# Kernel optimization log

Hardware: AMD Instinct MI355X
Metric: run time of the kernel (lower is better)

The kernel has to match this reference:

```python
import jax, jax.numpy as jnp
import numpy as np

SEQ, ATTN_LEN, C_IN, PS, DIM, LAYERS, HEADS, MLP = 10, 3, 48, 1, 48, 2, 8, 192


def setup_inputs() -> dict:
    key = jax.random.key(0)
    ks = jax.random.split(key, 10)
    B, H, W = 8, 64, 64
    s = 0.02
    f32 = jnp.float32
    return {
        "x": jax.random.normal(ks[0], (B, SEQ, C_IN, H, W), f32),
        "qkv_w": jax.random.normal(ks[1], (LAYERS, DIM, 3 * DIM), f32) * s,
        "qkv_b": jnp.zeros((LAYERS, 3 * DIM), f32),
        "proj_w": jax.random.normal(ks[2], (LAYERS, DIM, DIM), f32) * s,
        "proj_b": jnp.zeros((LAYERS, DIM), f32),
        "ff1_w": jax.random.normal(ks[3], (LAYERS, DIM, MLP), f32) * s,
        "ff1_b": jnp.zeros((LAYERS, MLP), f32),
        "ff2_w": jax.random.normal(ks[4], (LAYERS, MLP, DIM), f32) * s,
        "ff2_b": jnp.zeros((LAYERS, DIM), f32),
        "dw_w": jax.random.normal(ks[5], (2 * C_IN, 1, 3, 3), f32) * s,
        "dw_b": jnp.zeros((2 * C_IN,), f32),
        "ln_g": jnp.ones((2 * C_IN,), f32),
        "ln_b": jnp.zeros((2 * C_IN,), f32),
        "pw1_w": jax.random.normal(ks[6], (2 * C_IN, 8 * C_IN), f32) * s,
        "pw1_b": jnp.zeros((8 * C_IN,), f32),
        "pw2_w": jax.random.normal(ks[7], (8 * C_IN, C_IN), f32) * s,
        "pw2_b": jnp.zeros((C_IN,), f32),
        "sc_w": jax.random.normal(ks[8], (C_IN, 2 * C_IN), f32) * s,
        "sc_b": jnp.zeros((C_IN,), f32),
    }


def reference(x, qkv_w, qkv_b, proj_w, proj_b, ff1_w, ff1_b, ff2_w, ff2_b,
              dw_w, dw_b, ln_g, ln_b, pw1_w, pw1_b, pw2_w, pw2_b, sc_w, sc_b):
    B, C, F, H, W = x.shape
    # patchify (patch_size=1): (b, c, f, h, w) -> (b*h*w, c, f)
    t = x.transpose(0, 3, 4, 1, 2).reshape(B * H * W, C, F)
    # banded mask: True (disallowed) where |i-j| > attn_length//2
    nb = ATTN_LEN // 2
    idx = jnp.arange(C)
    mask = jnp.abs(idx[:, None] - idx[None, :]) > nb  # (C, C)
    neg = -jnp.finfo(t.dtype).max
    hd = DIM // HEADS
    scale = hd ** -0.5
    for l in range(LAYERS):
        # self-attention; NOTE: source computes scores = k @ q^T and softmaxes
        # over the query axis (faithful to original, not standard attention).
        qkv = (t @ qkv_w[l] + qkv_b[l]).reshape(B * H * W, C, 3, HEADS, hd)
        q, k, v = qkv[:, :, 0], qkv[:, :, 1], qkv[:, :, 2]  # (N, C, HEADS, hd)
        attn = jnp.einsum('nihd,njhd->nhij', k, q) * scale  # (N, HEADS, C, C)
        attn = jax.nn.softmax(jnp.where(mask, neg, attn), axis=-1)
        o = jnp.einsum('nhij,njhd->nihd', attn, v).reshape(B * H * W, C, DIM)
        t = t + (o @ proj_w[l] + proj_b[l])  # residual
        # feed-forward (GELU exact, as torch nn.GELU)
        h1 = jax.nn.gelu(t @ ff1_w[l] + ff1_b[l], approximate=False)
        t = t + (h1 @ ff2_w[l] + ff2_b[l])  # residual
    # unpatchify back to (B, C, F, H, W)
    y = t.reshape(B, H, W, C, F).transpose(0, 3, 4, 1, 2)
    # context_dropout is a no-op in eval with rate 0.0
    # concat original + context features along channels: (B*C, 2F, H, W)
    cat = jnp.concatenate([x.reshape(-1, F, H, W), y.reshape(-1, F, H, W)], axis=1)
    # ConvNeXt block: depthwise 3x3 -> channel LN -> pw expand -> GELU -> pw -> + 1x1 shortcut
    z = jax.lax.conv_general_dilated(cat, dw_w, (1, 1), 'SAME',
                                     feature_group_count=2 * F,
                                     dimension_numbers=('NCHW', 'OIHW', 'NCHW'))
    z = z + dw_b[None, :, None, None]
    z = z.transpose(0, 2, 3, 1)  # NHWC
    mu = z.mean(-1, keepdims=True)
    var = ((z - mu) ** 2).mean(-1, keepdims=True)
    z = (z - mu) / jnp.sqrt(var + 1e-6) * ln_g + ln_b
    z = jax.nn.gelu(z @ pw1_w + pw1_b, approximate=False) @ pw2_w + pw2_b
    z = z.transpose(0, 3, 1, 2)  # back to NCHW, F channels
    sc = jnp.einsum('nchw,oc->nohw', cat, sc_w) + sc_b[None, :, None, None]
    return (sc + z).reshape(B, C, F, H, W)
```

## Files before the change

kernel.cpp:

```cpp
#include <hip/hip_runtime.h>
#include <math.h>

#define THREADS 256


#define LKS 49

__global__ __launch_bounds__(64, 3) void ka2_transformer(
    const float* __restrict__ x,
    const float* __restrict__ qkv_w, const float* __restrict__ qkv_b,
    const float* __restrict__ proj_w, const float* __restrict__ proj_b,
    const float* __restrict__ ff1_w, const float* __restrict__ ff1_b,
    const float* __restrict__ ff2_w, const float* __restrict__ ff2_b,
    float* __restrict__ t_out)
{
    __shared__ float tl[64 * LKS];
    const int lane = threadIdx.x;

    const int nb  = gridDim.x;
    const int q8  = nb >> 3, r8 = nb & 7;
    const int xcd = blockIdx.x & 7, idx = blockIdx.x >> 3;
    const int wg  = (xcd < r8) ? xcd * (q8 + 1) + idx
                               : r8 * (q8 + 1) + (xcd - r8) * q8 + idx;

    const int s = lane / 10;
    const int c = lane - s * 10;
    const int g = wg * 6 + s;
    const bool act = (lane < 60) && (g < 32768);
    const int b   = g >> 12;
    const int pix = g & 4095;

    float* tr = tl + lane * LKS;

    if (act) {
        const float* xp = x + ((size_t)(b * 480 + c * 48)) * 4096 + pix;
        #pragma unroll
        for (int f = 0; f < 48; ++f) tr[f] = xp[(size_t)f * 4096];
    } else {
        #pragma unroll
        for (int f = 0; f < 48; ++f) tr[f] = 0.f;
    }

    const float scale = 0.4082482904638631f;
    const float NEG = -3.4e38f;

    for (int l = 0; l < 2; ++l) {
        const float* qw  = qkv_w + l * 6912;
        const float* qb  = qkv_b + l * 144;
        const float* pw  = proj_w + l * 2304;
        const float* pb  = proj_b + l * 48;
        const float* f1w = ff1_w + l * 9216;
        const float* f1b = ff1_b + l * 192;
        const float* f2w = ff2_w + l * 9216;
        const float* f2b = ff2_b + l * 48;

        float pacc[48];
        #pragma unroll
        for (int o = 0; o < 48; ++o) pacc[o] = 0.f;

        for (int h = 0; h < 8; ++h) {
            float qa[6], ka[6], va[6];
            #pragma unroll
            for (int d = 0; d < 6; ++d) { qa[d] = 0.f; ka[d] = 0.f; va[d] = 0.f; }

            for (int k = 0; k < 48; ++k) {
                const float tk = tr[k];
                const float* wr = qw + k * 144 + h * 6;
                #pragma unroll
                for (int d = 0; d < 6; ++d) {
                    qa[d] += tk * wr[d];
                    ka[d] += tk * wr[48 + d];
                    va[d] += tk * wr[96 + d];
                }
            }
            #pragma unroll
            for (int d = 0; d < 6; ++d) {
                qa[d] += qb[h * 6 + d];
                ka[d] += qb[48 + h * 6 + d];
                va[d] += qb[96 + h * 6 + d];
            }

            float qm[6], qp[6], vm[6], vp[6];
            #pragma unroll
            for (int d = 0; d < 6; ++d) {
                qm[d] = __shfl_up(qa[d], 1);
                qp[d] = __shfl_down(qa[d], 1);
                vm[d] = __shfl_up(va[d], 1);
                vp[d] = __shfl_down(va[d], 1);
            }
            float s0 = 0.f, sm = 0.f, sp = 0.f;
            #pragma unroll
            for (int d = 0; d < 6; ++d) {
                s0 += ka[d] * qa[d];
                sm += ka[d] * qm[d];
                sp += ka[d] * qp[d];
            }
            s0 *= scale; sm *= scale; sp *= scale;
            if (c == 0) sm = NEG;
            if (c == 9) sp = NEG;
            const float mx = fmaxf(s0, fmaxf(sm, sp));
            const float em = expf(sm - mx), e0 = expf(s0 - mx), ep = expf(sp - mx);
            const float inv = 1.0f / (em + e0 + ep);

            #pragma unroll
            for (int d = 0; d < 6; ++d) {
                const float ov = (em * vm[d] + e0 * va[d] + ep * vp[d]) * inv;
                const float* wr = pw + (h * 6 + d) * 48;
                #pragma unroll
                for (int o = 0; o < 48; ++o) pacc[o] += ov * wr[o];
            }
        }
        #pragma unroll
        for (int f = 0; f < 48; ++f) tr[f] += pacc[f] + pb[f];

        float facc[48];
        #pragma unroll
        for (int o = 0; o < 48; ++o) facc[o] = 0.f;

        for (int cc = 0; cc < 8; ++cc) {
            float ha[24];
            #pragma unroll
            for (int j = 0; j < 24; ++j) ha[j] = 0.f;

            for (int k = 0; k < 48; ++k) {
                const float tk = tr[k];
                const float* wr = f1w + k * 192 + cc * 24;
                #pragma unroll
                for (int j = 0; j < 24; ++j) ha[j] += tk * wr[j];
            }
            #pragma unroll
            for (int j = 0; j < 24; ++j) {
                float v = ha[j] + f1b[cc * 24 + j];
                ha[j] = 0.5f * v * (1.f + erff(v * 0.70710678118654752f));
            }
            #pragma unroll
            for (int j = 0; j < 24; ++j) {
                const float hj = ha[j];
                const float* wr = f2w + (cc * 24 + j) * 48;
                #pragma unroll
                for (int o = 0; o < 48; ++o) facc[o] += hj * wr[o];
            }
        }
        #pragma unroll
        for (int f = 0; f < 48; ++f) tr[f] += facc[f] + f2b[f];
    }

    if (act) {
        float* dst = t_out + (size_t)g * 480 + c * 48;
        #pragma unroll
        for (int u = 0; u < 12; ++u) {
            float4 v;
            v.x = tr[u * 4]; v.y = tr[u * 4 + 1];
            v.z = tr[u * 4 + 2]; v.w = tr[u * 4 + 3];
            *(float4*)(dst + u * 4) = v;
        }
    }
}

__global__ __launch_bounds__(THREADS) void kb_conv(
    const float* __restrict__ x, const float* __restrict__ t_in,
    const float* __restrict__ dw_w, const float* __restrict__ dw_b,
    float* __restrict__ z0)
{
    __shared__ float ct[100 * 97];
    const int tid = threadIdx.x;
    const int blk = blockIdx.x;
    const int n = blk >> 6;
    const int tile = blk & 63;
    const int th0 = (tile >> 3) << 3;
    const int tw0 = (tile & 7) << 3;
    const int b = n / 10, c = n % 10;

    for (int idx = tid; idx < 4800; idx += THREADS) {
        int f = idx / 100, p = idx % 100;
        int py = p / 10, px = p % 10;
        int gh = th0 + py - 1, gw = tw0 + px - 1;
        float v = 0.f;
        if ((unsigned)gh < 64u && (unsigned)gw < 64u)
            v = x[((size_t)n * 48 + f) * 4096 + gh * 64 + gw];
        ct[p * 97 + f] = v;
    }
    for (int idx = tid; idx < 4800; idx += THREADS) {
        int p = idx / 48, f = idx % 48;
        int py = p / 10, px = p % 10;
        int gh = th0 + py - 1, gw = tw0 + px - 1;
        float v = 0.f;
        if ((unsigned)gh < 64u && (unsigned)gw < 64u)
            v = t_in[(size_t)(b * 4096 + gh * 64 + gw) * 480 + c * 48 + f];
        ct[p * 97 + 48 + f] = v;
    }
    __syncthreads();

    #pragma unroll 4
    for (int it = 0; it < 24; ++it) {
        int oidx = tid + it * THREADS;
        int pxl = oidx / 96, ch = oidx % 96;
        int py = pxl >> 3, pxx = pxl & 7;
        const float* wp = dw_w + ch * 9;
        float acc = dw_b[ch];
        #pragma unroll
        for (int dy = 0; dy < 3; ++dy)
            #pragma unroll
            for (int dx = 0; dx < 3; ++dx)
                acc += ct[((py + dy) * 10 + pxx + dx) * 97 + ch] * wp[dy * 3 + dx];
        z0[((size_t)n * 4096 + (th0 + py) * 64 + (tw0 + pxx)) * 96 + ch] = acc;
    }
}

__global__ __launch_bounds__(THREADS, 3) void kc_mlp(
    const float* __restrict__ x, const float* __restrict__ t_in,
    const float* __restrict__ z0,
    const float* __restrict__ ln_g, const float* __restrict__ ln_b,
    const float* __restrict__ pw1_w, const float* __restrict__ pw1_b,
    const float* __restrict__ pw2_w, const float* __restrict__ pw2_b,
    const float* __restrict__ sc_w, const float* __restrict__ sc_b,
    float* __restrict__ out)
{
    __shared__ float zb[64 * 100];
    __shared__ float hb[64 * 100];
    const int tid = threadIdx.x;
    const int blk = blockIdx.x;
    const int n   = blk >> 6;
    const int hw0 = (blk & 63) << 6;
    const size_t pixbase = (size_t)n * 4096 + hw0;

    for (int idx = tid; idx < 1536; idx += THREADS) {
        float4 v = *(const float4*)(z0 + pixbase * 96 + (size_t)idx * 4);
        int p = idx / 24, c0 = (idx % 24) * 4;
        *(float4*)(&zb[p * 100 + c0]) = v;
    }
    __syncthreads();

    if (tid < 64) {
        float* r = zb + tid * 100;
        float mu = 0.f;
        #pragma unroll
        for (int k = 0; k < 96; ++k) mu += r[k];
        mu *= (1.f / 96.f);
        float var = 0.f;
        #pragma unroll
        for (int k = 0; k < 96; ++k) { float d = r[k] - mu; var += d * d; }
        var *= (1.f / 96.f);
        float rs = rsqrtf(var + 1e-6f);
        #pragma unroll
        for (int k = 0; k < 96; ++k) r[k] = (r[k] - mu) * rs * ln_g[k] + ln_b[k];
    }
    __syncthreads();

    const int pxg = tid >> 4;
    const int sub = tid & 15;
    const int f0  = sub * 3;

    float facc[4][3];
    #pragma unroll
    for (int r = 0; r < 4; ++r)
        #pragma unroll
        for (int c = 0; c < 3; ++c) facc[r][c] = pw2_b[f0 + c];

    for (int jc = 0; jc < 4; ++jc) {
        {
            const int j0 = jc * 96 + sub * 6;
            const float* zr = zb + pxg * 400;
            float h[4][6] = {};
            for (int k = 0; k < 96; k += 4) {
                float4 a0 = *(const float4*)(zr + k);
                float4 a1 = *(const float4*)(zr + 100 + k);
                float4 a2 = *(const float4*)(zr + 200 + k);
                float4 a3 = *(const float4*)(zr + 300 + k);
                #pragma unroll
                for (int kk = 0; kk < 4; ++kk) {
                    const float* wr = pw1_w + (k + kk) * 384 + j0;
                    const float e0 = (&a0.x)[kk], e1 = (&a1.x)[kk], e2 = (&a2.x)[kk], e3 = (&a3.x)[kk];
                    #pragma unroll
                    for (int c = 0; c < 6; ++c) {
                        const float w = wr[c];
                        h[0][c] += e0 * w; h[1][c] += e1 * w;
                        h[2][c] += e2 * w; h[3][c] += e3 * w;
                    }
                }
            }
            #pragma unroll
            for (int r = 0; r < 4; ++r)
                #pragma unroll
                for (int c = 0; c < 6; ++c) {
                    float v = h[r][c] + pw1_b[j0 + c];
                    v = 0.5f * v * (1.f + erff(v * 0.70710678118654752f));
                    hb[(pxg * 4 + r) * 100 + sub * 6 + c] = v;
                }
        }
        __syncthreads();

        {
            const float* hr = hb + pxg * 400;
            for (int k = 0; k < 96; k += 4) {
                float4 a0 = *(const float4*)(hr + k);
                float4 a1 = *(const float4*)(hr + 100 + k);
                float4 a2 = *(const float4*)(hr + 200 + k);
                float4 a3 = *(const float4*)(hr + 300 + k);
                #pragma unroll
                for (int kk = 0; kk < 4; ++kk) {
                    const float* wr = pw2_w + (jc * 96 + k + kk) * 48 + f0;
                    const float w0 = wr[0], w1 = wr[1], w2 = wr[2];
                    const float e0 = (&a0.x)[kk], e1 = (&a1.x)[kk], e2 = (&a2.x)[kk], e3 = (&a3.x)[kk];
                    facc[0][0] += e0 * w0; facc[0][1] += e0 * w1; facc[0][2] += e0 * w2;
                    facc[1][0] += e1 * w0; facc[1][1] += e1 * w1; facc[1][2] += e1 * w2;
                    facc[2][0] += e2 * w0; facc[2][1] += e2 * w1; facc[2][2] += e2 * w2;
                    facc[3][0] += e3 * w0; facc[3][1] += e3 * w1; facc[3][2] += e3 * w2;
                }
            }
        }
        __syncthreads();
    }

    for (int idx = tid; idx < 768; idx += THREADS) {
        int ch = idx >> 4, p0 = (idx & 15) << 2;
        float4 v = *(const float4*)(x + ((size_t)n * 48 + ch) * 4096 + hw0 + p0);
        zb[(p0 + 0) * 100 + ch] = v.x; zb[(p0 + 1) * 100 + ch] = v.y;
        zb[(p0 + 2) * 100 + ch] = v.z; zb[(p0 + 3) * 100 + ch] = v.w;
    }
    {
        const size_t tb = ((size_t)(n / 10) * 4096 + hw0);
        const int coff = (n % 10) * 48;
        for (int idx = tid; idx < 768; idx += THREADS) {
            int p = idx / 12, u0 = (idx % 12) * 4;
            float4 v = *(const float4*)(t_in + (tb + p) * 480 + coff + u0);
            *(float4*)(&zb[p * 100 + 48 + u0]) = v;
        }
    }
    __syncthreads();

    {
        const float* cr = zb + pxg * 400;
        for (int k = 0; k < 96; k += 4) {
            float4 a0 = *(const float4*)(cr + k);
            float4 a1 = *(const float4*)(cr + 100 + k);
            float4 a2 = *(const float4*)(cr + 200 + k);
            float4 a3 = *(const float4*)(cr + 300 + k);
            float4 w0 = *(const float4*)(sc_w + (f0 + 0) * 96 + k);
            float4 w1 = *(const float4*)(sc_w + (f0 + 1) * 96 + k);
            float4 w2 = *(const float4*)(sc_w + (f0 + 2) * 96 + k);
            #pragma unroll
            for (int kk = 0; kk < 4; ++kk) {
                const float e0 = (&a0.x)[kk], e1 = (&a1.x)[kk], e2 = (&a2.x)[kk], e3 = (&a3.x)[kk];
                const float q0 = (&w0.x)[kk], q1 = (&w1.x)[kk], q2 = (&w2.x)[kk];
                facc[0][0] += e0 * q0; facc[0][1] += e0 * q1; facc[0][2] += e0 * q2;
                facc[1][0] += e1 * q0; facc[1][1] += e1 * q1; facc[1][2] += e1 * q2;
                facc[2][0] += e2 * q0; facc[2][1] += e2 * q1; facc[2][2] += e2 * q2;
                facc[3][0] += e3 * q0; facc[3][1] += e3 * q1; facc[3][2] += e3 * q2;
            }
        }
    }
    __syncthreads();

    #pragma unroll
    for (int r = 0; r < 4; ++r)
        #pragma unroll
        for (int c = 0; c < 3; ++c)
            hb[(f0 + c) * 66 + pxg * 4 + r] = facc[r][c] + sc_b[f0 + c];
    __syncthreads();
    for (int idx = tid; idx < 768; idx += THREADS) {
        int f = idx / 16, p0 = (idx % 16) * 4;
        float4 v;
        v.x = hb[f * 66 + p0]; v.y = hb[f * 66 + p0 + 1];
        v.z = hb[f * 66 + p0 + 2]; v.w = hb[f * 66 + p0 + 3];
        *(float4*)(out + ((size_t)n * 48 + f) * 4096 + hw0 + p0) = v;
    }
}

extern "C" void kernel_launch(void* const* d_in, const int* in_sizes, int n_in,
                              void* d_out, int out_size, void* d_ws, size_t ws_size,
                              hipStream_t stream) {
    const float* x      = (const float*)d_in[0];
    const float* qkv_w  = (const float*)d_in[1];
    const float* qkv_b  = (const float*)d_in[2];
    const float* proj_w = (const float*)d_in[3];
    const float* proj_b = (const float*)d_in[4];
    const float* ff1_w  = (const float*)d_in[5];
    const float* ff1_b  = (const float*)d_in[6];
    const float* ff2_w  = (const float*)d_in[7];
    const float* ff2_b  = (const float*)d_in[8];
    const float* dw_w   = (const float*)d_in[9];
    const float* dw_b   = (const float*)d_in[10];
    const float* ln_g   = (const float*)d_in[11];
    const float* ln_b   = (const float*)d_in[12];
    const float* pw1_w  = (const float*)d_in[13];
    const float* pw1_b  = (const float*)d_in[14];
    const float* pw2_w  = (const float*)d_in[15];
    const float* pw2_b  = (const float*)d_in[16];
    const float* sc_w   = (const float*)d_in[17];
    const float* sc_b   = (const float*)d_in[18];
    float* out = (float*)d_out;

    float* t_out = (float*)d_ws;
    float* z0    = t_out + 15728640ull;

    ka2_transformer<<<5462, 64, 0, stream>>>(x, qkv_w, qkv_b, proj_w, proj_b,
                                             ff1_w, ff1_b, ff2_w, ff2_b, t_out);
    kb_conv<<<5120, THREADS, 0, stream>>>(x, t_out, dw_w, dw_b, z0);
    kc_mlp<<<5120, THREADS, 0, stream>>>(x, t_out, z0, ln_g, ln_b,
                                         pw1_w, pw1_b, pw2_w, pw2_b, sc_w, sc_b, out);
}
```

Measured before the change: 1.981 ms.

## Rewrite pointwise MLP kernel as one-pixel-per-lane single-wave blocks with register accumulators

The ConvNeXt MLP kernel now uses 64-thread blocks where each lane owns one pixel. Each lane keeps all 48 output accumulators in registers and streams the hidden layer through in 24-wide chunks, so the shared hidden buffer and the barriers inside the loop are gone. Weights are read with wave-uniform addresses, which should let them become scalar or broadcast loads. A small pre-kernel transposes the shortcut weights into a device global so they can be read the same way. The cost is heavy register pressure (48 plus 24 accumulators) and only one wave per block, which may lower occupancy or cause spills.

```diff
diff --git a/kernel.cpp b/kernel.cpp
--- a/kernel.cpp
+++ b/kernel.cpp
@@ -3,6 +3,16 @@
 
 #define THREADS 256
 
+
+__device__ float g_scwT[96 * 48];
+
+__global__ void kt_transpose(const float* __restrict__ sc_w) {
+    int i = threadIdx.x + blockIdx.x * 256;
+    if (i < 48 * 96) {
+        int o = i / 96, k = i % 96;
+        g_scwT[k * 48 + o] = sc_w[o * 96 + k];
+    }
+}
 
 #define LKS 49
 
@@ -207,163 +217,126 @@
     }
 }
 
-__global__ __launch_bounds__(THREADS, 3) void kc_mlp(
+#define ZS 100
+
+__global__ __launch_bounds__(64) void kc2_mlp(
     const float* __restrict__ x, const float* __restrict__ t_in,
     const float* __restrict__ z0,
     const float* __restrict__ ln_g, const float* __restrict__ ln_b,
     const float* __restrict__ pw1_w, const float* __restrict__ pw1_b,
     const float* __restrict__ pw2_w, const float* __restrict__ pw2_b,
-    const float* __restrict__ sc_w, const float* __restrict__ sc_b,
+    const float* __restrict__ sc_b,
     float* __restrict__ out)
 {
-    __shared__ float zb[64 * 100];
-    __shared__ float hb[64 * 100];
-    const int tid = threadIdx.x;
+    __shared__ float zb[64 * ZS];
+    const int lane = threadIdx.x;
     const int blk = blockIdx.x;
     const int n   = blk >> 6;
     const int hw0 = (blk & 63) << 6;
     const size_t pixbase = (size_t)n * 4096 + hw0;
 
-    for (int idx = tid; idx < 1536; idx += THREADS) {
+    for (int idx = lane; idx < 1536; idx += 64) {
         float4 v = *(const float4*)(z0 + pixbase * 96 + (size_t)idx * 4);
         int p = idx / 24, c0 = (idx % 24) * 4;
-        *(float4*)(&zb[p * 100 + c0]) = v;
+        *(float4*)(&zb[p * ZS + c0]) = v;
     }
     __syncthreads();
 
-    if (tid < 64) {
-        float* r = zb + tid * 100;
+    float* zr = zb + lane * ZS;
+
+    {
         float mu = 0.f;
-        #pragma unroll
-        for (int k = 0; k < 96; ++k) mu += r[k];
+        for (int k = 0; k < 96; k += 4) {
+            float4 v = *(const float4*)(zr + k);
+            mu += v.x; mu += v.y; mu += v.z; mu += v.w;
+        }
         mu *= (1.f / 96.f);
         float var = 0.f;
-        #pragma unroll
-        for (int k = 0; k < 96; ++k) { float d = r[k] - mu; var += d * d; }
+        for (int k = 0; k < 96; k += 4) {
+            float4 v = *(const float4*)(zr + k);
+            float d0 = v.x - mu, d1 = v.y - mu, d2 = v.z - mu, d3 = v.w - mu;
+            var += d0 * d0; var += d1 * d1; var += d2 * d2; var += d3 * d3;
+        }
         var *= (1.f / 96.f);
         float rs = rsqrtf(var + 1e-6f);
-        #pragma unroll
-        for (int k = 0; k < 96; ++k) r[k] = (r[k] - mu) * rs * ln_g[k] + ln_b[k];
-    }
+        for (int k = 0; k < 96; k += 4) {
+            float4 v = *(const float4*)(zr + k);
+            v.x = (v.x - mu) * rs * ln_g[k + 0] + ln_b[k + 0];
+            v.y = (v.y - mu) * rs * ln_g[k + 1] + ln_b[k + 1];
+            v.z = (v.z - mu) * rs * ln_g[k + 2] + ln_b[k + 2];
+            v.w = (v.w - mu) * rs * ln_g[k + 3] + ln_b[k + 3];
+            *(float4*)(zr + k) = v;
+        }
+    }
+
+    float facc[48];
+    #pragma unroll
+    for (int o = 0; o < 48; ++o) facc[o] = pw2_b[o];
+
+    for (int jc = 0; jc < 16; ++jc) {
+        const int j0 = jc * 24;
+        float ha[24];
+        #pragma unroll
+        for (int j = 0; j < 24; ++j) ha[j] = 0.f;
+
+        for (int k = 0; k < 96; k += 4) {
+            float4 a = *(const float4*)(zr + k);
+            #pragma unroll
+            for (int kk = 0; kk < 4; ++kk) {
+                const float e = (&a.x)[kk];
+                const float* wr = pw1_w + (k + kk) * 384 + j0;
+                #pragma unroll
+                for (int j = 0; j < 24; ++j) ha[j] += e * wr[j];
+            }
+        }
+        #pragma unroll
+        for (int j = 0; j < 24; ++j) {
+            float v = ha[j] + pw1_b[j0 + j];
+            ha[j] = 0.5f * v * (1.f + erff(v * 0.70710678118654752f));
+        }
+        #pragma unroll
+        for (int j = 0; j < 24; ++j) {
+            const float hj = ha[j];
+            const float* wr = pw2_w + (j0 + j) * 48;
+            #pragma unroll
+            for (int o = 0; o < 48; ++o) facc[o] += hj * wr[o];
+        }
+    }
+
     __syncthreads();
-
-    const int pxg = tid >> 4;
-    const int sub = tid & 15;
-    const int f0  = sub * 3;
-
-    float facc[4][3];
-    #pragma unroll
-    for (int r = 0; r < 4; ++r)
-        #pragma unroll
-        for (int c = 0; c < 3; ++c) facc[r][c] = pw2_b[f0 + c];
-
-    for (int jc = 0; jc < 4; ++jc) {
-        {
-            const int j0 = jc * 96 + sub * 6;
-            const float* zr = zb + pxg * 400;
-            float h[4][6] = {};
-            for (int k = 0; k < 96; k += 4) {
-                float4 a0 = *(const float4*)(zr + k);
-                float4 a1 = *(const float4*)(zr + 100 + k);
-                float4 a2 = *(const float4*)(zr + 200 + k);
-                float4 a3 = *(const float4*)(zr + 300 + k);
-                #pragma unroll
-                for (int kk = 0; kk < 4; ++kk) {
-                    const float* wr = pw1_w + (k + kk) * 384 + j0;
-                    const float e0 = (&a0.x)[kk], e1 = (&a1.x)[kk], e2 = (&a2.x)[kk], e3 = (&a3.x)[kk];
-                    #pragma unroll
-                    for (int c = 0; c < 6; ++c) {
-                        const float w = wr[c];
-                        h[0][c] += e0 * w; h[1][c] += e1 * w;
-                        h[2][c] += e2 * w; h[3][c] += e3 * w;
-                    }
-                }
-            }
-            #pragma unroll
-            for (int r = 0; r < 4; ++r)
-                #pragma unroll
-                for (int c = 0; c < 6; ++c) {
-                    float v = h[r][c] + pw1_b[j0 + c];
-                    v = 0.5f * v * (1.f + erff(v * 0.70710678118654752f));
-                    hb[(pxg * 4 + r) * 100 + sub * 6 + c] = v;
-                }
-        }
-        __syncthreads();
-
-        {
-            const float* hr = hb + pxg * 400;
-            for (int k = 0; k < 96; k += 4) {
-                float4 a0 = *(const float4*)(hr + k);
-                float4 a1 = *(const float4*)(hr + 100 + k);
-                float4 a2 = *(const float4*)(hr + 200 + k);
-                float4 a3 = *(const float4*)(hr + 300 + k);
-                #pragma unroll
-                for (int kk = 0; kk < 4; ++kk) {
-                    const float* wr = pw2_w + (jc * 96 + k + kk) * 48 + f0;
-                    const float w0 = wr[0], w1 = wr[1], w2 = wr[2];
-                    const float e0 = (&a0.x)[kk], e1 = (&a1.x)[kk], e2 = (&a2.x)[kk], e3 = (&a3.x)[kk];
-                    facc[0][0] += e0 * w0; facc[0][1] += e0 * w1; facc[0][2] += e0 * w2;
-                    facc[1][0] += e1 * w0; facc[1][1] += e1 * w1; facc[1][2] += e1 * w2;
-                    facc[2][0] += e2 * w0; facc[2][1] += e2 * w1; facc[2][2] += e2 * w2;
-                    facc[3][0] += e3 * w0; facc[3][1] += e3 * w1; facc[3][2] += e3 * w2;
-                }
-            }
-        }
-        __syncthreads();
-    }
-
-    for (int idx = tid; idx < 768; idx += THREADS) {
+    for (int idx = lane; idx < 768; idx += 64) {
         int ch = idx >> 4, p0 = (idx & 15) << 2;
         float4 v = *(const float4*)(x + ((size_t)n * 48 + ch) * 4096 + hw0 + p0);
-        zb[(p0 + 0) * 100 + ch] = v.x; zb[(p0 + 1) * 100 + ch] = v.y;
-        zb[(p0 + 2) * 100 + ch] = v.z; zb[(p0 + 3) * 100 + ch] = v.w;
+        zb[(p0 + 0) * ZS + ch] = v.x; zb[(p0 + 1) * ZS + ch] = v.y;
+        zb[(p0 + 2) * ZS + ch] = v.z; zb[(p0 + 3) * ZS + ch] = v.w;
     }
     {
         const size_t tb = ((size_t)(n / 10) * 4096 + hw0);
         const int coff = (n % 10) * 48;
-        for (int idx = tid; idx < 768; idx += THREADS) {
+        for (int idx = lane; idx < 768; idx += 64) {
             int p = idx / 12, u0 = (idx % 12) * 4;
             float4 v = *(const float4*)(t_in + (tb + p) * 480 + coff + u0);
-            *(float4*)(&zb[p * 100 + 48 + u0]) = v;
+            *(float4*)(&zb[p * ZS + 48 + u0]) = v;
         }
     }
     __syncthreads();
 
+    for (int k = 0; k < 96; k += 4) {
+        float4 a = *(const float4*)(zr + k);
+        #pragma unroll
+        for (int kk = 0; kk < 4; ++kk) {
+            const float e = (&a.x)[kk];
+            const float* wr = g_scwT + (k + kk) * 48;
+            #pragma unroll
+            for (int o = 0; o < 48; ++o) facc[o] += e * wr[o];
+        }
+    }
+
     {
-        const float* cr = zb + pxg * 400;
-        for (int k = 0; k < 96; k += 4) {
-            float4 a0 = *(const float4*)(cr + k);
-            float4 a1 = *(const float4*)(cr + 100 + k);
-            float4 a2 = *(const float4*)(cr + 200 + k);
-            float4 a3 = *(const float4*)(cr + 300 + k);
-            float4 w0 = *(const float4*)(sc_w + (f0 + 0) * 96 + k);
-            float4 w1 = *(const float4*)(sc_w + (f0 + 1) * 96 + k);
-            float4 w2 = *(const float4*)(sc_w + (f0 + 2) * 96 + k);
-            #pragma unroll
-            for (int kk = 0; kk < 4; ++kk) {
-                const float e0 = (&a0.x)[kk], e1 = (&a1.x)[kk], e2 = (&a2.x)[kk], e3 = (&a3.x)[kk];
-                const float q0 = (&w0.x)[kk], q1 = (&w1.x)[kk], q2 = (&w2.x)[kk];
-                facc[0][0] += e0 * q0; facc[0][1] += e0 * q1; facc[0][2] += e0 * q2;
-                facc[1][0] += e1 * q0; facc[1][1] += e1 * q1; facc[1][2] += e1 * q2;
-                facc[2][0] += e2 * q0; facc[2][1] += e2 * q1; facc[2][2] += e2 * q2;
-                facc[3][0] += e3 * q0; facc[3][1] += e3 * q1; facc[3][2] += e3 * q2;
-            }
-        }
-    }
-    __syncthreads();
-
-    #pragma unroll
-    for (int r = 0; r < 4; ++r)
-        #pragma unroll
-        for (int c = 0; c < 3; ++c)
-            hb[(f0 + c) * 66 + pxg * 4 + r] = facc[r][c] + sc_b[f0 + c];
-    __syncthreads();
-    for (int idx = tid; idx < 768; idx += THREADS) {
-        int f = idx / 16, p0 = (idx % 16) * 4;
-        float4 v;
-        v.x = hb[f * 66 + p0]; v.y = hb[f * 66 + p0 + 1];
-        v.z = hb[f * 66 + p0 + 2]; v.w = hb[f * 66 + p0 + 3];
-        *(float4*)(out + ((size_t)n * 48 + f) * 4096 + hw0 + p0) = v;
+        float* op = out + (size_t)n * 48 * 4096 + hw0 + lane;
+        #pragma unroll
+        for (int f = 0; f < 48; ++f)
+            op[(size_t)f * 4096] = facc[f] + sc_b[f];
     }
 }
 
@@ -394,9 +367,10 @@
     float* t_out = (float*)d_ws;
     float* z0    = t_out + 15728640ull;
 
+    kt_transpose<<<18, 256, 0, stream>>>(sc_w);
     ka2_transformer<<<5462, 64, 0, stream>>>(x, qkv_w, qkv_b, proj_w, proj_b,
                                              ff1_w, ff1_b, ff2_w, ff2_b, t_out);
     kb_conv<<<5120, THREADS, 0, stream>>>(x, t_out, dw_w, dw_b, z0);
-    kc_mlp<<<5120, THREADS, 0, stream>>>(x, t_out, z0, ln_g, ln_b,
-                                         pw1_w, pw1_b, pw2_w, pw2_b, sc_w, sc_b, out);
-}
+    kc2_mlp<<<5120, 64, 0, stream>>>(x, t_out, z0, ln_g, ln_b,
+                                     pw1_w, pw1_b, pw2_w, pw2_b, sc_b, out);
+}
```

Measured after the change: 3.333 ms. 68.2% more time.
